# Performance work log

Hardware: AMD Instinct MI355X
Metric: run time of the kernel (lower is better)

Reference implementation:

```python
import jax, jax.numpy as jnp
import numpy as np

B, T, N, F_IN, F_OUT, K = 4, 32, 1024, 128, 128, 4


def setup_inputs() -> dict:
    key = jax.random.key(0)
    k1, k2, k3 = jax.random.split(key, 3)
    X = jax.random.normal(k1, (B, T, N, F_IN), dtype=jnp.float32)
    # graph-shift operator; 1/sqrt(N) scaling keeps S^k products numerically tame
    S = jax.random.normal(k2, (N, N), dtype=jnp.float32) / np.float32(np.sqrt(N))
    W = jax.random.normal(k3, (F_OUT, F_IN, K), dtype=jnp.float32) * 0.1
    b = jnp.zeros((F_OUT,), dtype=jnp.float32)
    return {"X": X, "S": S, "W": W, "b": b}


def reference(X, S, W, b):
    # Y[:, t] = sum_{k=0}^{K-1, t-k>=0} S^k @ X[:, t-k] @ W[:, :, k]^T + b
    # (static graph: the per-(t,k) shift-chain product in the original collapses to S^k)
    Bsz, Tlen, Nn, Fin = X.shape
    Kord = W.shape[-1]
    Y = jnp.zeros((Bsz, Tlen, Nn, W.shape[0]), X.dtype)
    Z = X  # Z = S^k @ X, starting at k=0 (identity)
    for k in range(Kord):
        # causal time-shift by k: output at t uses Z at t-k (zeros for t-k<0)
        Zs = Z if k == 0 else jnp.pad(Z, ((0, 0), (k, 0), (0, 0), (0, 0)))[:, :Tlen]
        Y = Y + jnp.einsum('btnf,of->btno', Zs, W[:, :, k])
        if k < Kord - 1:
            Z = jnp.einsum('nm,btmf->btnf', S, Z)  # advance shift power
    return Y + b
```

## Files before the change

kernel.cpp:

```cpp
#include <hip/hip_runtime.h>
#include <stdint.h>

#define BT 128
#define NN 1024
#define FF 128

typedef __attribute__((ext_vector_type(8))) short short8;
typedef __attribute__((ext_vector_type(4))) float float4v;
typedef __attribute__((ext_vector_type(4))) unsigned short ushort4v;

__device__ __forceinline__ unsigned short f2bf(float f) {
  uint32_t u = __builtin_bit_cast(uint32_t, f);
  u += 0x7FFFu + ((u >> 16) & 1u);
  return (unsigned short)(u >> 16);
}

__device__ __forceinline__ void gload16(const void* g, void* l) {
  __builtin_amdgcn_global_load_lds(
      (const __attribute__((address_space(1))) uint32_t*)(g),
      (__attribute__((address_space(3))) uint32_t*)(l),
      16, 0, 0);
}

__global__ __launch_bounds__(256) void k_cvt_sw(const float* __restrict__ S,
                                                unsigned short* __restrict__ Sbf,
                                                const float* __restrict__ W,
                                                unsigned short* __restrict__ Wk2,
                                                unsigned short* __restrict__ zbuf) {
  int tid = threadIdx.x;
  int b = blockIdx.x;
  if (b < 64) {
#pragma unroll
    for (int i = 0; i < 16; ++i) {
      int g4 = b * 4096 + i * 256 + tid;
      float4v v = reinterpret_cast<const float4v*>(S)[g4];
      ushort4v h;
      h[0] = f2bf(v[0]); h[1] = f2bf(v[1]); h[2] = f2bf(v[2]); h[3] = f2bf(v[3]);
      reinterpret_cast<ushort4v*>(Sbf)[g4] = h;
    }
  } else if (b < 320) {
    int gid = (b - 64) * 256 + tid;
    int k = gid >> 14, o = (gid >> 7) & 127, f = gid & 127;
    Wk2[gid] = f2bf(W[(o * 128 + f) * 4 + k]);
  } else {
    ushort4v z = (ushort4v){0, 0, 0, 0};
#pragma unroll
    for (int i = 0; i < 16; ++i)
      reinterpret_cast<ushort4v*>(zbuf)[(b - 320) * 4096 + i * 256 + tid] = z;
  }
}

__global__ __launch_bounds__(256) void k_cvt_x(const float* __restrict__ X,
                                               unsigned short* __restrict__ Xbf) {
  int base = blockIdx.x * 1024 + threadIdx.x;
#pragma unroll
  for (int i = 0; i < 4; ++i) {
    int g4 = base + i * 256;
    float4v v = reinterpret_cast<const float4v*>(X)[g4];
    ushort4v h;
    h[0] = f2bf(v[0]); h[1] = f2bf(v[1]); h[2] = f2bf(v[2]); h[3] = f2bf(v[3]);
    reinterpret_cast<ushort4v*>(Xbf)[g4] = h;
  }
}

__global__ __launch_bounds__(256) void k_proj(const unsigned short* __restrict__ Wk2,
                                              const unsigned short* __restrict__ Xbf,
                                              unsigned short* __restrict__ U3) {
  __shared__ unsigned short lA[128 * 64];
  __shared__ unsigned short lB[128 * 64];
  int bt = blockIdx.x >> 3;
  int n0 = (blockIdx.x & 7) << 7;
  int tid = threadIdx.x;
  int wave = tid >> 6, lane = tid & 63;
  int wr = wave >> 1, wc = wave & 1;
  int lr = lane & 15, g = lane >> 4;

  const unsigned short* gA = Wk2 + 3 * (FF * FF);
  const unsigned short* gB = Xbf + (size_t)bt * (NN * FF) + (size_t)n0 * FF;

  float4v acc[4][4];
#pragma unroll
  for (int a = 0; a < 4; ++a)
#pragma unroll
    for (int b = 0; b < 4; ++b) acc[a][b] = (float4v){0.f, 0.f, 0.f, 0.f};

  for (int kt = 0; kt < 2; ++kt) {
    int m0 = kt * 64;
#pragma unroll
    for (int i = 0; i < 4; ++i) {
      int id = i * 256 + tid;
      int row = id >> 3;
      int mc = (id & 7) << 3;
      int slot = (i * 256 + (tid & 192)) * 8;
      gload16(gA + (size_t)row * 128 + m0 + mc, &lA[slot]);
      gload16(gB + (size_t)row * 128 + m0 + mc, &lB[slot]);
    }
    __syncthreads();
#pragma unroll
    for (int kk = 0; kk < 2; ++kk) {
      short8 aF[4], bF[4];
#pragma unroll
      for (int mi = 0; mi < 4; ++mi)
        aF[mi] = *reinterpret_cast<const short8*>(
            &lA[(wr * 64 + mi * 16 + lr) * 64 + kk * 32 + g * 8]);
#pragma unroll
      for (int ni = 0; ni < 4; ++ni)
        bF[ni] = *reinterpret_cast<const short8*>(
            &lB[(wc * 64 + ni * 16 + lr) * 64 + kk * 32 + g * 8]);
#pragma unroll
      for (int mi = 0; mi < 4; ++mi)
#pragma unroll
        for (int ni = 0; ni < 4; ++ni)
          acc[mi][ni] = __builtin_amdgcn_mfma_f32_16x16x32_bf16(
              aF[mi], bF[ni], acc[mi][ni], 0, 0, 0);
    }
    __syncthreads();
  }

  unsigned short* Uo = U3 + (size_t)bt * (NN * FF);
#pragma unroll
  for (int mi = 0; mi < 4; ++mi) {
#pragma unroll
    for (int ni = 0; ni < 4; ++ni) {
      int o = wr * 64 + mi * 16 + g * 4;
      int n = n0 + wc * 64 + ni * 16 + lr;
#pragma unroll
      for (int j = 0; j < 4; ++j)
        Uo[(size_t)(o + j) * NN + n] = f2bf(acc[mi][ni][j]);
    }
  }
}

template <bool FINAL>
__global__ __launch_bounds__(1024, 4) void k_chain(
    const unsigned short* __restrict__ Uin,
    const unsigned short* __restrict__ Sbf,
    const unsigned short* __restrict__ Wg,
    const unsigned short* __restrict__ Xbf,
    const unsigned short* __restrict__ zbuf,
    unsigned short* __restrict__ Hout,
    float* __restrict__ Yout,
    const float* __restrict__ bias) {
  extern __shared__ unsigned char lds[];

  int bid = blockIdx.x;
  int logical = (bid & 7) * 32 + (bid >> 3);
  int cblk = logical >> 2;
  int nblk = logical & 3;

  int tid = threadIdx.x;
  int wave = tid >> 6, lane = tid & 63;
  int wave_m = wave >> 2, wave_n = wave & 3;
  int lr = lane & 15, g = lane >> 4;

  const int bt0 = cblk * 2;
  const bool t0z = ((bt0 & 31) == 0);
  const unsigned short* A0 = t0z ? zbuf : (Uin + (size_t)(bt0 - 1) * (NN * FF));
  const unsigned short* A1 = Uin + (size_t)bt0 * (NN * FF);

  const int rbe = ((wave * 8) & 31) + ((wave >> 2) << 6);
  const unsigned laneOff = (unsigned)((lane >> 3) * NN) +
                           (unsigned)(((lane & 7) ^ ((lane >> 3) & 7)) << 3);
  const unsigned short* baseAe =
      (wave < 8) ? (A0 + (size_t)rbe * NN) : (A1 + (size_t)(rbe - 128) * NN);
  const unsigned short* baseAo = baseAe + 32 * NN;
  const unsigned short* baseBe = Sbf + (size_t)(nblk * 256 + rbe) * NN;
  const unsigned short* baseBo = baseBe + 32 * NN;
  const unsigned dAe = (unsigned)rbe * 128u;
  const unsigned dAo = dAe + 4096u;
  const unsigned dBe = 32768u + (unsigned)rbe * 128u;
  const unsigned dBo = dBe + 4096u;

  const unsigned xm = (unsigned)((lr & 7) << 4);
  const unsigned xo0 = ((unsigned)(g * 16)) ^ xm;
  const unsigned xo1 = ((unsigned)(64 + g * 16)) ^ xm;
  const unsigned aRB = (unsigned)((wave_m * 64 + lr) * 128);
  const unsigned bRB = 32768u + (unsigned)((wave_n * 64 + lr) * 128);

#define RD(OFF) (*reinterpret_cast<const short8*>(lds + (OFF)))

  float4v acc[4][4];
#pragma unroll
  for (int a = 0; a < 4; ++a)
#pragma unroll
    for (int b = 0; b < 4; ++b) acc[a][b] = (float4v){0.f, 0.f, 0.f, 0.f};

  short8 aF[2], bF[4];

  gload16(baseBe + laneOff, lds + dBe);
  gload16(baseBo + laneOff, lds + dBo);
  gload16(baseAe + laneOff, lds + dAe);
  gload16(baseAo + laneOff, lds + dAo);
  asm volatile("s_waitcnt vmcnt(0)" ::: "memory");
  __builtin_amdgcn_s_barrier();

  for (int kt = 0; kt < 16; ++kt) {
    const unsigned bo = (unsigned)(kt & 1) << 16;
    const unsigned nbo = bo ^ 65536u;
    const unsigned ko = (unsigned)(kt + 1) * 64u;
    const bool st = (kt < 15);

    aF[0] = RD(bo + aRB + xo0);
    aF[1] = RD(bo + aRB + 2048u + xo0);
#pragma unroll
    for (int nf = 0; nf < 4; ++nf) bF[nf] = RD(bo + bRB + (unsigned)nf * 2048u + xo0);
    if (st) {
      gload16(baseBe + laneOff + ko, lds + nbo + dBe);
      asm volatile("s_waitcnt vmcnt(1)" ::: "memory");
    } else {
      asm volatile("s_waitcnt vmcnt(0)" ::: "memory");
    }
    __builtin_amdgcn_s_barrier();
    asm volatile("s_waitcnt lgkmcnt(0)" ::: "memory");
    __builtin_amdgcn_sched_barrier(0);
    __builtin_amdgcn_s_setprio(1);
#pragma unroll
    for (int nf = 0; nf < 4; ++nf) {
      acc[0][nf] = __builtin_amdgcn_mfma_f32_16x16x32_bf16(aF[0], bF[nf], acc[0][nf], 0, 0, 0);
      acc[1][nf] = __builtin_amdgcn_mfma_f32_16x16x32_bf16(aF[1], bF[nf], acc[1][nf], 0, 0, 0);
    }
    __builtin_amdgcn_s_setprio(0);
    __builtin_amdgcn_sched_barrier(0);
    __builtin_amdgcn_s_barrier();
    __builtin_amdgcn_sched_barrier(0);

    aF[0] = RD(bo + aRB + 4096u + xo0);
    aF[1] = RD(bo + aRB + 6144u + xo0);
    if (st) gload16(baseBo + laneOff + ko, lds + nbo + dBo);
    __builtin_amdgcn_s_barrier();
    asm volatile("s_waitcnt lgkmcnt(0)" ::: "memory");
    __builtin_amdgcn_sched_barrier(0);
    __builtin_amdgcn_s_setprio(1);
#pragma unroll
    for (int nf = 0; nf < 4; ++nf) {
      acc[2][nf] = __builtin_amdgcn_mfma_f32_16x16x32_bf16(aF[0], bF[nf], acc[2][nf], 0, 0, 0);
      acc[3][nf] = __builtin_amdgcn_mfma_f32_16x16x32_bf16(aF[1], bF[nf], acc[3][nf], 0, 0, 0);
    }
    __builtin_amdgcn_s_setprio(0);
    __builtin_amdgcn_sched_barrier(0);
    __builtin_amdgcn_s_barrier();
    __builtin_amdgcn_sched_barrier(0);

    aF[0] = RD(bo + aRB + xo1);
    aF[1] = RD(bo + aRB + 2048u + xo1);
#pragma unroll
    for (int nf = 0; nf < 4; ++nf) bF[nf] = RD(bo + bRB + (unsigned)nf * 2048u + xo1);
    if (st) gload16(baseAe + laneOff + ko, lds + nbo + dAe);
    __builtin_amdgcn_s_barrier();
    asm volatile("s_waitcnt lgkmcnt(0)" ::: "memory");
    __builtin_amdgcn_sched_barrier(0);
    __builtin_amdgcn_s_setprio(1);
#pragma unroll
    for (int nf = 0; nf < 4; ++nf) {
      acc[0][nf] = __builtin_amdgcn_mfma_f32_16x16x32_bf16(aF[0], bF[nf], acc[0][nf], 0, 0, 0);
      acc[1][nf] = __builtin_amdgcn_mfma_f32_16x16x32_bf16(aF[1], bF[nf], acc[1][nf], 0, 0, 0);
    }
    __builtin_amdgcn_s_setprio(0);
    __builtin_amdgcn_sched_barrier(0);
    __builtin_amdgcn_s_barrier();
    __builtin_amdgcn_sched_barrier(0);

    aF[0] = RD(bo + aRB + 4096u + xo1);
    aF[1] = RD(bo + aRB + 6144u + xo1);
    if (st) {
      gload16(baseAo + laneOff + ko, lds + nbo + dAo);
      asm volatile("s_waitcnt vmcnt(1)" ::: "memory");
    }
    __builtin_amdgcn_s_barrier();
    asm volatile("s_waitcnt lgkmcnt(0)" ::: "memory");
    __builtin_amdgcn_sched_barrier(0);
    __builtin_amdgcn_s_setprio(1);
#pragma unroll
    for (int nf = 0; nf < 4; ++nf) {
      acc[2][nf] = __builtin_amdgcn_mfma_f32_16x16x32_bf16(aF[0], bF[nf], acc[2][nf], 0, 0, 0);
      acc[3][nf] = __builtin_amdgcn_mfma_f32_16x16x32_bf16(aF[1], bF[nf], acc[3][nf], 0, 0, 0);
    }
    __builtin_amdgcn_s_setprio(0);
    __builtin_amdgcn_sched_barrier(0);
    __builtin_amdgcn_s_barrier();
    __builtin_amdgcn_sched_barrier(0);
  }
#undef RD

  const int bt = bt0 + (wave_m >> 1);
  const int oh = (wave_m & 1) * 64;
  const unsigned short* Xb = Xbf + (size_t)bt * (NN * FF);
  const int nbase = nblk * 256 + wave_n * 64;
#pragma unroll 1
  for (int kk = 0; kk < 4; ++kk) {
    int fc = kk * 32 + g * 8;
    short8 aW[4], bW[4];
#pragma unroll
    for (int mf = 0; mf < 4; ++mf)
      aW[mf] = *reinterpret_cast<const short8*>(Wg + (size_t)(oh + mf * 16 + lr) * FF + fc);
#pragma unroll
    for (int nf = 0; nf < 4; ++nf)
      bW[nf] = *reinterpret_cast<const short8*>(Xb + (size_t)(nbase + nf * 16 + lr) * FF + fc);
#pragma unroll
    for (int mf = 0; mf < 4; ++mf)
#pragma unroll
      for (int nf = 0; nf < 4; ++nf)
        acc[mf][nf] = __builtin_amdgcn_mfma_f32_16x16x32_bf16(aW[mf], bW[nf], acc[mf][nf], 0, 0, 0);
  }

  if constexpr (FINAL) {
    float* Yp = Yout + (size_t)bt * (NN * FF);
#pragma unroll
    for (int mf = 0; mf < 4; ++mf) {
      int o0 = oh + mf * 16 + g * 4;
      float4v bv = *reinterpret_cast<const float4v*>(bias + o0);
#pragma unroll
      for (int nf = 0; nf < 4; ++nf) {
        int n = nbase + nf * 16 + lr;
        float4v r = acc[mf][nf] + bv;
        *reinterpret_cast<float4v*>(Yp + (size_t)n * FF + o0) = r;
      }
    }
  } else {
    unsigned short* Hp = Hout + (size_t)bt * (NN * FF);
#pragma unroll
    for (int mf = 0; mf < 4; ++mf) {
      int o0 = oh + mf * 16 + g * 4;
#pragma unroll
      for (int nf = 0; nf < 4; ++nf) {
        int n = nbase + nf * 16 + lr;
#pragma unroll
        for (int j = 0; j < 4; ++j)
          Hp[(size_t)(o0 + j) * NN + n] = f2bf(acc[mf][nf][j]);
      }
    }
  }
}


extern "C" void kernel_launch(void* const* d_in, const int* in_sizes, int n_in,
                              void* d_out, int out_size, void* d_ws, size_t ws_size,
                              hipStream_t stream) {
  const float* X = (const float*)d_in[0];
  const float* S = (const float*)d_in[1];
  const float* W = (const float*)d_in[2];
  const float* bvec = (const float*)d_in[3];
  float* Y = (float*)d_out;

  char* ws = (char*)d_ws;
  const size_t ZB = (size_t)BT * NN * FF * sizeof(unsigned short);
  unsigned short* Xbf = (unsigned short*)(ws + 0 * ZB);
  unsigned short* U3  = (unsigned short*)(ws + 1 * ZB);
  unsigned short* H2  = (unsigned short*)(ws + 2 * ZB);
  unsigned short* H1  = (unsigned short*)(ws + 3 * ZB);
  unsigned short* Sbf = (unsigned short*)(ws + 4 * ZB);
  unsigned short* Wk2 = (unsigned short*)(ws + 4 * ZB + (size_t)2097152);
  unsigned short* zbf = (unsigned short*)(ws + 4 * ZB + (size_t)2097152 + 131072);

  k_cvt_sw<<<dim3(328), dim3(256), 0, stream>>>(S, Sbf, W, Wk2, zbf);
  k_cvt_x<<<dim3(4096), dim3(256), 0, stream>>>(X, Xbf);
  k_proj<<<dim3(1024), dim3(256), 0, stream>>>(Wk2, Xbf, U3);

  hipError_t e0 = hipFuncSetAttribute((const void*)k_chain<false>,
                      hipFuncAttributeMaxDynamicSharedMemorySize, 131072);
  hipError_t e1 = hipFuncSetAttribute((const void*)k_chain<true>,
                      hipFuncAttributeMaxDynamicSharedMemorySize, 131072);
  (void)e0; (void)e1;

  k_chain<false><<<dim3(256), dim3(1024), 131072, stream>>>(
      U3, Sbf, Wk2 + 2 * (FF * FF), Xbf, zbf, H2, nullptr, nullptr);
  k_chain<false><<<dim3(256), dim3(1024), 131072, stream>>>(
      H2, Sbf, Wk2 + 1 * (FF * FF), Xbf, zbf, H1, nullptr, nullptr);
  k_chain<true><<<dim3(256), dim3(1024), 131072, stream>>>(
      H1, Sbf, Wk2, Xbf, zbf, nullptr, Y, bvec);
}
```

Before: 184.3 us.

## Shrink chain-kernel tiles to one timestep per 512-thread block with 4-stage pipeline

The chain GEMM kernel now has each 512-thread block handle one timestep (128 rows) against a 256-column slice of S, where it previously handled two timesteps with 1024 threads. The grid doubles to 512 blocks. The K loop uses 32-wide k-steps with a four-buffer LDS ring and prefetch two steps ahead. This replaces the old 64-wide double buffer that interleaved four loads per step, and the XOR swizzle is dropped. The aim is more blocks for better CU balance and less LDS per block, at the cost of reloading the S tile once per timestep instead of sharing it across two, and possible LDS bank conflicts without the swizzle.

```diff
diff --git a/kernel.cpp b/kernel.cpp
--- a/kernel.cpp
+++ b/kernel.cpp
@@ -132,7 +132,7 @@
 }
 
 template <bool FINAL>
-__global__ __launch_bounds__(1024, 4) void k_chain(
+__global__ __launch_bounds__(512, 2) void k_chain(
     const unsigned short* __restrict__ Uin,
     const unsigned short* __restrict__ Sbf,
     const unsigned short* __restrict__ Wg,
@@ -144,7 +144,7 @@
   extern __shared__ unsigned char lds[];
 
   int bid = blockIdx.x;
-  int logical = (bid & 7) * 32 + (bid >> 3);
+  int logical = (bid & 7) * 64 + (bid >> 3);
   int cblk = logical >> 2;
   int nblk = logical & 3;
 
@@ -153,29 +153,21 @@
   int wave_m = wave >> 2, wave_n = wave & 3;
   int lr = lane & 15, g = lane >> 4;
 
-  const int bt0 = cblk * 2;
-  const bool t0z = ((bt0 & 31) == 0);
-  const unsigned short* A0 = t0z ? zbuf : (Uin + (size_t)(bt0 - 1) * (NN * FF));
-  const unsigned short* A1 = Uin + (size_t)bt0 * (NN * FF);
-
-  const int rbe = ((wave * 8) & 31) + ((wave >> 2) << 6);
-  const unsigned laneOff = (unsigned)((lane >> 3) * NN) +
-                           (unsigned)(((lane & 7) ^ ((lane >> 3) & 7)) << 3);
-  const unsigned short* baseAe =
-      (wave < 8) ? (A0 + (size_t)rbe * NN) : (A1 + (size_t)(rbe - 128) * NN);
-  const unsigned short* baseAo = baseAe + 32 * NN;
-  const unsigned short* baseBe = Sbf + (size_t)(nblk * 256 + rbe) * NN;
-  const unsigned short* baseBo = baseBe + 32 * NN;
-  const unsigned dAe = (unsigned)rbe * 128u;
-  const unsigned dAo = dAe + 4096u;
-  const unsigned dBe = 32768u + (unsigned)rbe * 128u;
-  const unsigned dBo = dBe + 4096u;
-
-  const unsigned xm = (unsigned)((lr & 7) << 4);
-  const unsigned xo0 = ((unsigned)(g * 16)) ^ xm;
-  const unsigned xo1 = ((unsigned)(64 + g * 16)) ^ xm;
-  const unsigned aRB = (unsigned)((wave_m * 64 + lr) * 128);
-  const unsigned bRB = 32768u + (unsigned)((wave_n * 64 + lr) * 128);
+  const int bt = cblk;
+  const unsigned short* A = ((bt & 31) == 0) ? zbuf
+                            : (Uin + (size_t)(bt - 1) * (NN * FF));
+
+  const int srow = tid >> 2;
+  const int sseg = tid & 3;
+  const unsigned short* srcA = A + (size_t)srow * NN + sseg * 8;
+  const unsigned short* srcB0 = Sbf + (size_t)(nblk * 256 + srow) * NN + sseg * 8;
+  const unsigned short* srcB1 = srcB0 + (size_t)128 * NN;
+  const unsigned dA = (unsigned)(tid * 16);
+  const unsigned dB0 = 8192u + (unsigned)(tid * 16);
+  const unsigned dB1 = 16384u + (unsigned)(tid * 16);
+
+  const unsigned aRB = (unsigned)((wave_m * 64 + lr) * 64 + g * 16);
+  const unsigned bRB = 8192u + (unsigned)((wave_n * 64 + lr) * 64 + g * 16);
 
 #define RD(OFF) (*reinterpret_cast<const short8*>(lds + (OFF)))
 
@@ -185,29 +177,34 @@
 #pragma unroll
     for (int b = 0; b < 4; ++b) acc[a][b] = (float4v){0.f, 0.f, 0.f, 0.f};
 
-  short8 aF[2], bF[4];
-
-  gload16(baseBe + laneOff, lds + dBe);
-  gload16(baseBo + laneOff, lds + dBo);
-  gload16(baseAe + laneOff, lds + dAe);
-  gload16(baseAo + laneOff, lds + dAo);
-  asm volatile("s_waitcnt vmcnt(0)" ::: "memory");
+  short8 aF[4], bF[4];
+
+  gload16(srcA, lds + dA);
+  gload16(srcB0, lds + dB0);
+  gload16(srcB1, lds + dB1);
+  gload16(srcA + 32, lds + 24576 + dA);
+  gload16(srcB0 + 32, lds + 24576 + dB0);
+  gload16(srcB1 + 32, lds + 24576 + dB1);
+  asm volatile("s_waitcnt vmcnt(3)" ::: "memory");
   __builtin_amdgcn_s_barrier();
 
-  for (int kt = 0; kt < 16; ++kt) {
-    const unsigned bo = (unsigned)(kt & 1) << 16;
-    const unsigned nbo = bo ^ 65536u;
-    const unsigned ko = (unsigned)(kt + 1) * 64u;
-    const bool st = (kt < 15);
-
-    aF[0] = RD(bo + aRB + xo0);
-    aF[1] = RD(bo + aRB + 2048u + xo0);
-#pragma unroll
-    for (int nf = 0; nf < 4; ++nf) bF[nf] = RD(bo + bRB + (unsigned)nf * 2048u + xo0);
-    if (st) {
-      gload16(baseBe + laneOff + ko, lds + nbo + dBe);
-      asm volatile("s_waitcnt vmcnt(1)" ::: "memory");
-    } else {
+#pragma unroll 4
+  for (int kt = 0; kt < 32; ++kt) {
+    const unsigned bo = (unsigned)(kt & 3) * 24576u;
+
+#pragma unroll
+    for (int mf = 0; mf < 4; ++mf) aF[mf] = RD(bo + aRB + (unsigned)mf * 1024u);
+#pragma unroll
+    for (int nf = 0; nf < 4; ++nf) bF[nf] = RD(bo + bRB + (unsigned)nf * 1024u);
+
+    if (kt < 30) {
+      const unsigned nbo = (unsigned)((kt + 2) & 3) * 24576u;
+      const unsigned ko = (unsigned)(kt + 2) * 32u;
+      gload16(srcA + ko, lds + nbo + dA);
+      gload16(srcB0 + ko, lds + nbo + dB0);
+      gload16(srcB1 + ko, lds + nbo + dB1);
+      asm volatile("s_waitcnt vmcnt(3)" ::: "memory");
+    } else if (kt == 30) {
       asm volatile("s_waitcnt vmcnt(0)" ::: "memory");
     }
     __builtin_amdgcn_s_barrier();
@@ -215,75 +212,19 @@
     __builtin_amdgcn_sched_barrier(0);
     __builtin_amdgcn_s_setprio(1);
 #pragma unroll
-    for (int nf = 0; nf < 4; ++nf) {
-      acc[0][nf] = __builtin_amdgcn_mfma_f32_16x16x32_bf16(aF[0], bF[nf], acc[0][nf], 0, 0, 0);
-      acc[1][nf] = __builtin_amdgcn_mfma_f32_16x16x32_bf16(aF[1], bF[nf], acc[1][nf], 0, 0, 0);
-    }
+    for (int mf = 0; mf < 4; ++mf)
+#pragma unroll
+      for (int nf = 0; nf < 4; ++nf)
+        acc[mf][nf] = __builtin_amdgcn_mfma_f32_16x16x32_bf16(
+            aF[mf], bF[nf], acc[mf][nf], 0, 0, 0);
     __builtin_amdgcn_s_setprio(0);
     __builtin_amdgcn_sched_barrier(0);
     __builtin_amdgcn_s_barrier();
     __builtin_amdgcn_sched_barrier(0);
-
-    aF[0] = RD(bo + aRB + 4096u + xo0);
-    aF[1] = RD(bo + aRB + 6144u + xo0);
-    if (st) gload16(baseBo + laneOff + ko, lds + nbo + dBo);
-    __builtin_amdgcn_s_barrier();
-    asm volatile("s_waitcnt lgkmcnt(0)" ::: "memory");
-    __builtin_amdgcn_sched_barrier(0);
-    __builtin_amdgcn_s_setprio(1);
-#pragma unroll
-    for (int nf = 0; nf < 4; ++nf) {
-      acc[2][nf] = __builtin_amdgcn_mfma_f32_16x16x32_bf16(aF[0], bF[nf], acc[2][nf], 0, 0, 0);
-      acc[3][nf] = __builtin_amdgcn_mfma_f32_16x16x32_bf16(aF[1], bF[nf], acc[3][nf], 0, 0, 0);
-    }
-    __builtin_amdgcn_s_setprio(0);
-    __builtin_amdgcn_sched_barrier(0);
-    __builtin_amdgcn_s_barrier();
-    __builtin_amdgcn_sched_barrier(0);
-
-    aF[0] = RD(bo + aRB + xo1);
-    aF[1] = RD(bo + aRB + 2048u + xo1);
-#pragma unroll
-    for (int nf = 0; nf < 4; ++nf) bF[nf] = RD(bo + bRB + (unsigned)nf * 2048u + xo1);
-    if (st) gload16(baseAe + laneOff + ko, lds + nbo + dAe);
-    __builtin_amdgcn_s_barrier();
-    asm volatile("s_waitcnt lgkmcnt(0)" ::: "memory");
-    __builtin_amdgcn_sched_barrier(0);
-    __builtin_amdgcn_s_setprio(1);
-#pragma unroll
-    for (int nf = 0; nf < 4; ++nf) {
-      acc[0][nf] = __builtin_amdgcn_mfma_f32_16x16x32_bf16(aF[0], bF[nf], acc[0][nf], 0, 0, 0);
-      acc[1][nf] = __builtin_amdgcn_mfma_f32_16x16x32_bf16(aF[1], bF[nf], acc[1][nf], 0, 0, 0);
-    }
-    __builtin_amdgcn_s_setprio(0);
-    __builtin_amdgcn_sched_barrier(0);
-    __builtin_amdgcn_s_barrier();
-    __builtin_amdgcn_sched_barrier(0);
-
-    aF[0] = RD(bo + aRB + 4096u + xo1);
-    aF[1] = RD(bo + aRB + 6144u + xo1);
-    if (st) {
-      gload16(baseAo + laneOff + ko, lds + nbo + dAo);
-      asm volatile("s_waitcnt vmcnt(1)" ::: "memory");
-    }
-    __builtin_amdgcn_s_barrier();
-    asm volatile("s_waitcnt lgkmcnt(0)" ::: "memory");
-    __builtin_amdgcn_sched_barrier(0);
-    __builtin_amdgcn_s_setprio(1);
-#pragma unroll
-    for (int nf = 0; nf < 4; ++nf) {
-      acc[2][nf] = __builtin_amdgcn_mfma_f32_16x16x32_bf16(aF[0], bF[nf], acc[2][nf], 0, 0, 0);
-      acc[3][nf] = __builtin_amdgcn_mfma_f32_16x16x32_bf16(aF[1], bF[nf], acc[3][nf], 0, 0, 0);
-    }
-    __builtin_amdgcn_s_setprio(0);
-    __builtin_amdgcn_sched_barrier(0);
-    __builtin_amdgcn_s_barrier();
-    __builtin_amdgcn_sched_barrier(0);
   }
 #undef RD
 
-  const int bt = bt0 + (wave_m >> 1);
-  const int oh = (wave_m & 1) * 64;
+  const int oh = wave_m * 64;
   const unsigned short* Xb = Xbf + (size_t)bt * (NN * FF);
   const int nbase = nblk * 256 + wave_n * 64;
 #pragma unroll 1
@@ -357,15 +298,15 @@
   k_proj<<<dim3(1024), dim3(256), 0, stream>>>(Wk2, Xbf, U3);
 
   hipError_t e0 = hipFuncSetAttribute((const void*)k_chain<false>,
-                      hipFuncAttributeMaxDynamicSharedMemorySize, 131072);
+                      hipFuncAttributeMaxDynamicSharedMemorySize, 98304);
   hipError_t e1 = hipFuncSetAttribute((const void*)k_chain<true>,
-                      hipFuncAttributeMaxDynamicSharedMemorySize, 131072);
+                      hipFuncAttributeMaxDynamicSharedMemorySize, 98304);
   (void)e0; (void)e1;
 
-  k_chain<false><<<dim3(256), dim3(1024), 131072, stream>>>(
+  k_chain<false><<<dim3(512), dim3(512), 98304, stream>>>(
       U3, Sbf, Wk2 + 2 * (FF * FF), Xbf, zbf, H2, nullptr, nullptr);
-  k_chain<false><<<dim3(256), dim3(1024), 131072, stream>>>(
+  k_chain<false><<<dim3(512), dim3(512), 98304, stream>>>(
       H2, Sbf, Wk2 + 1 * (FF * FF), Xbf, zbf, H1, nullptr, nullptr);
-  k_chain<true><<<dim3(256), dim3(1024), 131072, stream>>>(
+  k_chain<true><<<dim3(512), dim3(512), 98304, stream>>>(
       H1, Sbf, Wk2, Xbf, zbf, nullptr, Y, bvec);
 }
```

Result: slower. 216.3 us (+17.4%).
